# Kernel tuning notes

Measured on AMD Instinct MI355X. Metric: run time of the kernel, lower is better.

The kernel has to match this reference:

```python
import jax, jax.numpy as jnp
import numpy as np

OPTION_NUM = 5
HEADS = 4
NUM_LAYERS = 3
N_NODES = 20000
N_EDGES = 640000
NODES_PER_GRAPH = 800
N_GRAPHS = 25          # N_NODES // NODES_PER_GRAPH, multiple of OPTION_NUM
N_GROUPS = 5           # N_GRAPHS // OPTION_NUM; must equal OPTION_NUM for output_layer
T_TOK = 256
TOKEN_DIM = 1024
D = 256                # out_channels
VOCAB = 100000


def setup_inputs() -> dict:
    key = jax.random.key(0)
    ks = jax.random.split(key, 16)
    nrm = lambda k, s: jax.random.normal(k, s, dtype=jnp.float32) * 0.05
    L = NUM_LAYERS
    return {
        "concept_ids": jax.random.randint(ks[0], (N_NODES,), 0, VOCAB, dtype=jnp.int32),
        "edge_index": jax.random.randint(ks[1], (2, N_EDGES), 0, N_NODES, dtype=jnp.int32),
        "edge_type": jax.random.randint(ks[2], (N_EDGES,), 0, 38, dtype=jnp.int32),
        "sentence_embeddings": nrm(ks[3], (N_GROUPS, TOKEN_DIM)),
        "token_embedding": nrm(ks[4], (N_GROUPS, T_TOK, TOKEN_DIM)),
        "batch": (jnp.arange(N_NODES, dtype=jnp.int32) // NODES_PER_GRAPH),
        "entity_embeddings": nrm(ks[5], (VOCAB, D)),
        "Wq": nrm(ks[6], (L, D, D)), "bq": jnp.zeros((L, D), jnp.float32),
        "Wk": nrm(ks[7], (L, D, D)), "bk": jnp.zeros((L, D), jnp.float32),
        "Wv": nrm(ks[8], (L, D, D)), "bv": jnp.zeros((L, D), jnp.float32),
        "Ws": nrm(ks[9], (L, TOKEN_DIM, D)), "bs": jnp.zeros((L, D), jnp.float32),
        "Wo": nrm(ks[10], (L, D, D)), "bo": jnp.zeros((L, D), jnp.float32),
        "W1": nrm(ks[11], (D, D)), "b1": jnp.zeros((D,), jnp.float32),
        "W2": nrm(ks[12], (TOKEN_DIM, D)), "b2": jnp.zeros((D,), jnp.float32),
        "W3": nrm(ks[13], (D, TOKEN_DIM)), "b3": jnp.zeros((TOKEN_DIM,), jnp.float32),
        "Wout": nrm(ks[14], (OPTION_NUM * D, D)), "bout": jnp.zeros((D,), jnp.float32),
    }


def reference(concept_ids, edge_index, edge_type, sentence_embeddings, token_embedding,
              batch, entity_embeddings, Wq, bq, Wk, bk, Wv, bv, Ws, bs, Wo, bo,
              W1, b1, W2, b2, W3, b3, Wout, bout):
    H = HEADS
    C = D // H
    sqdk = jnp.sqrt(jnp.float32(C))
    group = batch // OPTION_NUM                      # [N] in [0, N_GROUPS)
    row, col = edge_index[0], edge_index[1]

    x = entity_embeddings[concept_ids]               # [N, D]
    for l in range(NUM_LAYERS):
        Q = (x @ Wq[l] + bq[l]).reshape(-1, H, C)
        K = (x @ Wk[l] + bk[l]).reshape(-1, H, C)
        V = (x @ Wv[l] + bv[l]).reshape(-1, H, C)
        QS = (sentence_embeddings[group] @ Ws[l] + bs[l]).reshape(-1, H, C)
        Qi, Kj = Q[row], K[col]                      # [E, H, C]
        alpha = ((Qi * Kj).sum(-1) + (QS[row] * Kj).sum(-1) + (Qi * QS[col]).sum(-1)) / (3.0 * sqdk)
        alpha = jax.nn.leaky_relu(alpha, 0.2)
        alpha = jax.nn.softmax(alpha, axis=0)        # global softmax over edges (as in source)
        agg = jnp.zeros_like(V).at[row].add(V[col] * alpha[:, :, None])
        x = agg.reshape(-1, H * C) @ Wo[l] + bo[l] + x

    x = x @ W1 + b1                                  # [N, D]
    tok = token_embedding @ W2 + b2                  # [G, T, D]

    # attention_multihead (faithful double gather by group indices)
    scale = jnp.sqrt(jnp.float32(D))
    scores = jnp.einsum('nd,btd->bnt', x, tok) / scale   # [G, N, T]
    sel = scores[:, group, :]                            # gather dim 1
    w = jax.nn.softmax(sel, axis=-1)
    ao = jnp.einsum('bnt,btd->bnd', w, tok)              # [G, N, D]
    sel2 = ao[:, group, :]                               # second gather
    concat = jnp.transpose(sel2, (1, 0, 2)).reshape(x.shape[0], -1)  # [N, G*D]
    x = concat @ Wout + bout                             # [N, D]

    pooled = jax.ops.segment_max(x, batch, num_segments=N_GRAPHS)    # global_max_pool
    soft = pooled @ W3 + b3                              # [N_GRAPHS, token_dim]
    return soft.reshape(N_GRAPHS // OPTION_NUM, OPTION_NUM, -1)
```

## Files before the change

kernel.cpp:

```cpp
#include <hip/hip_runtime.h>
#include <hip/hip_bf16.h>

#define NNODES 20000
#define NEDGES 640000
#define DM 256
#define PAD 128

typedef short s16x8 __attribute__((ext_vector_type(8)));
typedef float f32x4 __attribute__((ext_vector_type(4)));
typedef float f32x2 __attribute__((ext_vector_type(2)));

__device__ inline float b2f(unsigned short u) {
  union { unsigned int i; float f; } z;
  z.i = (unsigned int)u << 16;
  return z.f;
}
__device__ inline unsigned short f2b(float f) {
  union { unsigned int i; float f; } z;
  z.f = f;
  unsigned int i = z.i;
  return (unsigned short)((i + 0x7FFFu + ((i >> 16) & 1u)) >> 16);
}

__device__ inline unsigned char f2fp8(float v) {
#if __has_builtin(__builtin_amdgcn_cvt_pk_fp8_f32)
  int t = __builtin_amdgcn_cvt_pk_fp8_f32(v, v, 0, false);
  return (unsigned char)(t & 0xFF);
#else
  union { float f; unsigned int u; } z;
  z.f = v;
  unsigned int s = (z.u >> 31) << 7;
  float av = fabsf(v);
  if (av >= 448.f) return (unsigned char)(s | 0x7E);
  if (av < 0.015625f) {
    int q = (int)rintf(av * 512.f);
    return (unsigned char)(s | (unsigned)q);
  }
  int e32 = (int)((z.u >> 23) & 255) - 127;
  unsigned mant = z.u & 0x7FFFFF;
  unsigned t = mant + 0x7FFFF + ((mant >> 20) & 1);
  if (t >= 0x800000u) { t = 0; e32++; }
  int e4 = e32 + 7;
  unsigned m3 = (t >> 20) & 7;
  if (e4 > 15 || (e4 == 15 && m3 == 7)) return (unsigned char)(s | 0x7E);
  return (unsigned char)(s | (unsigned)((e4 << 3) | m3));
#endif
}

__device__ inline float4 fp8x4_dec(unsigned int u) {
#if __has_builtin(__builtin_amdgcn_cvt_pk_f32_fp8)
  f32x2 lo = __builtin_amdgcn_cvt_pk_f32_fp8((int)u, false);
  f32x2 hi = __builtin_amdgcn_cvt_pk_f32_fp8((int)u, true);
  float4 r;
  r.x = lo[0]; r.y = lo[1]; r.z = hi[0]; r.w = hi[1];
  return r;
#else
  float4 r;
  float* p = &r.x;
#pragma unroll
  for (int j = 0; j < 4; j++) {
    unsigned b = (u >> (8 * j)) & 0xFF;
    unsigned s = b >> 7, e = (b >> 3) & 15, m = b & 7;
    float mag;
    if (e == 0) mag = (float)m * 0.001953125f;
    else {
      union { unsigned int i; float f; } z;
      z.i = ((e + 120u) << 23) | (m << 20);
      mag = z.f;
    }
    p[j] = s ? -mag : mag;
  }
  return r;
#endif
}

__global__ __launch_bounds__(256) void init_kernel(
    const int* __restrict__ cid, const float* __restrict__ ent,
    float* __restrict__ x, unsigned short* __restrict__ xb,
    const float* __restrict__ Wq, const float* __restrict__ Wk,
    const float* __restrict__ Wv, const float* __restrict__ Wo,
    unsigned short* __restrict__ WT, const float* __restrict__ W2,
    unsigned short* __restrict__ W2T, const float* __restrict__ te,
    unsigned short* __restrict__ tb, const float* __restrict__ sent,
    const float* __restrict__ Ws, const float* __restrict__ bs,
    float* __restrict__ QS5all, const int* __restrict__ ei,
    const int* __restrict__ batch, int* __restrict__ deg,
    int* __restrict__ colPad) {
  int blk = blockIdx.x;
  int j = threadIdx.x;
  if (blk < 60) {
    int chunk = blk & 3;
    int lg = blk >> 2;
    int l = lg / 5, g = lg % 5;
    __shared__ float sh[256];
    sh[j] = sent[g * 1024 + chunk * 256 + j];
    __syncthreads();
    const float* W = Ws + (size_t)l * 1024 * 256 + (size_t)chunk * 256 * 256;
    float acc = (chunk == 0) ? bs[l * 256 + j] : 0.f;
#pragma unroll 8
    for (int k = 0; k < 256; k++) acc += sh[k] * W[k * 256 + j];
    atomicAdd(&QS5all[(size_t)lg * 256 + j], acc);
  } else if (blk < 2560) {
    int e = (blk - 60) * 256 + j;
    if (e >= NEDGES) return;
    int r = ei[e];
    int c = ei[NEDGES + e];
    int slot = atomicAdd(&deg[r], 1);
    if (slot < PAD)
      colPad[(size_t)r * PAD + slot] = c | ((batch[c] / 5) << 24);
  } else if (blk < 7560) {
    int idx = (blk - 2560) * 256 + j;
    if (idx >= NNODES * 64) return;
    int node = idx >> 6, d4 = idx & 63;
    float4 v =
        reinterpret_cast<const float4*>(ent)[(size_t)cid[node] * 64 + d4];
    reinterpret_cast<float4*>(x)[(size_t)node * 64 + d4] = v;
    ushort4 b;
    b.x = f2b(v.x); b.y = f2b(v.y); b.z = f2b(v.z); b.w = f2b(v.w);
    reinterpret_cast<ushort4*>(xb)[(size_t)node * 64 + d4] = b;
  } else if (blk < 10632) {
    int pblk = blk - 7560;
    int slot = pblk >> 8;
    int l = slot >> 2, t = slot & 3;
    int n = pblk & 255;
    const float* src = (t == 0) ? Wq : (t == 1) ? Wk : (t == 2) ? Wv : Wo;
    WT[(size_t)slot * 65536 + n * 256 + j] =
        f2b(src[(size_t)l * 65536 + j * 256 + n]);
  } else if (blk < 11656) {
    int i = (blk - 10632) * 256 + j;
    int n = i >> 10, k = i & 1023;
    W2T[n * 1024 + k] = f2b(W2[k * 256 + n]);
  } else {
    int i = (blk - 11656) * 256 + j;
    float4 v = reinterpret_cast<const float4*>(te)[i];
    ushort4 b;
    b.x = f2b(v.x); b.y = f2b(v.y); b.z = f2b(v.z); b.w = f2b(v.w);
    reinterpret_cast<ushort4*>(tb)[i] = b;
  }
}

template <int WITH_TOK>
__global__ __launch_bounds__(256) void qkv_gemm_kernel(
    const unsigned short* __restrict__ A, const unsigned short* __restrict__ Bt,
    const float* __restrict__ bq, const float* __restrict__ bk,
    const float* __restrict__ bv, unsigned short* __restrict__ Qb,
    unsigned char* __restrict__ KV8, int M,
    const unsigned short* __restrict__ tokA,
    const unsigned short* __restrict__ W2T, const float* __restrict__ b2,
    float* __restrict__ tokOut) {
  int wid = threadIdx.x >> 6;
  int lane = threadIdx.x & 63;
  int wr = wid >> 1, wc = wid & 1;
  int r16 = lane & 15, kg = lane >> 4;
  if (WITH_TOK && blockIdx.x >= 6) {
    if (blockIdx.y >= 20) return;
    int rowBase = blockIdx.y * 64 + wr * 32;
    int colBase = (blockIdx.x - 6) * 128 + wc * 64;
    f32x4 acc[2][4] = {};
    for (int k0 = 0; k0 < 1024; k0 += 32) {
      s16x8 a[2], b[4];
#pragma unroll
      for (int mi = 0; mi < 2; mi++) {
        int r = rowBase + mi * 16 + r16;
        a[mi] = *reinterpret_cast<const s16x8*>(
            &tokA[(size_t)r * 1024 + k0 + kg * 8]);
      }
#pragma unroll
      for (int ni = 0; ni < 4; ni++) {
        int c = colBase + ni * 16 + r16;
        b[ni] = *reinterpret_cast<const s16x8*>(
            &W2T[(size_t)c * 1024 + k0 + kg * 8]);
      }
#pragma unroll
      for (int mi = 0; mi < 2; mi++)
#pragma unroll
        for (int ni = 0; ni < 4; ni++)
          acc[mi][ni] = __builtin_amdgcn_mfma_f32_16x16x32_bf16(
              a[mi], b[ni], acc[mi][ni], 0, 0, 0);
    }
#pragma unroll
    for (int mi = 0; mi < 2; mi++)
#pragma unroll
      for (int ni = 0; ni < 4; ni++) {
        int c = colBase + ni * 16 + (lane & 15);
        float bia = b2[c];
#pragma unroll
        for (int reg = 0; reg < 4; reg++) {
          int r = rowBase + mi * 16 + (lane >> 4) * 4 + reg;
          tokOut[(size_t)r * 256 + c] = acc[mi][ni][reg] + bia;
        }
      }
    return;
  }
  int rowBase = blockIdx.y * 64 + wr * 32;
  int colBase = blockIdx.x * 128 + wc * 64;
  f32x4 acc[2][4] = {};
  for (int k0 = 0; k0 < 256; k0 += 32) {
    s16x8 a[2], b[4];
#pragma unroll
    for (int mi = 0; mi < 2; mi++) {
      int r = rowBase + mi * 16 + r16;
      s16x8 z = {};
      a[mi] = (r < M) ? *reinterpret_cast<const s16x8*>(
                            &A[(size_t)r * 256 + k0 + kg * 8])
                      : z;
    }
#pragma unroll
    for (int ni = 0; ni < 4; ni++) {
      int c = colBase + ni * 16 + r16;
      b[ni] = *reinterpret_cast<const s16x8*>(&Bt[(size_t)c * 256 + k0 + kg * 8]);
    }
#pragma unroll
    for (int mi = 0; mi < 2; mi++)
#pragma unroll
      for (int ni = 0; ni < 4; ni++)
        acc[mi][ni] = __builtin_amdgcn_mfma_f32_16x16x32_bf16(
            a[mi], b[ni], acc[mi][ni], 0, 0, 0);
  }
  int region = (blockIdx.x * 128) >> 8;
  const float* bias = (region == 0) ? bq : (region == 1) ? bk : bv;
  unsigned char* dstBase = KV8 + ((region == 1) ? 0 : 256);
#pragma unroll
  for (int mi = 0; mi < 2; mi++)
#pragma unroll
    for (int ni = 0; ni < 4; ni++) {
      int cg = colBase + ni * 16 + (lane & 15);
      int cr = cg & 255;
      float bia = bias[cr];
#pragma unroll
      for (int reg = 0; reg < 4; reg++) {
        int r = rowBase + mi * 16 + (lane >> 4) * 4 + reg;
        if (r >= M) continue;
        float v = acc[mi][ni][reg] + bia;
        if (region == 0)
          Qb[(size_t)r * 256 + cr] = f2b(v);
        else
          dstBase[(size_t)r * 512 + cr] = f2fp8(v);
      }
    }
}

__global__ __launch_bounds__(256) void gemm_bf16_kernel(
    const unsigned short* __restrict__ A, const unsigned short* __restrict__ Bt,
    const float* __restrict__ bias, const float* __restrict__ resid,
    float* __restrict__ Cf, unsigned short* __restrict__ Cb, int M, int K) {
  int wid = threadIdx.x >> 6;
  int lane = threadIdx.x & 63;
  int wr = wid >> 1, wc = wid & 1;
  int rowBase = blockIdx.y * 64 + wr * 32;
  int colBase = blockIdx.x * 128 + wc * 64;
  int r16 = lane & 15, kg = lane >> 4;
  f32x4 acc[2][4] = {};
  for (int k0 = 0; k0 < K; k0 += 32) {
    s16x8 a[2], b[4];
#pragma unroll
    for (int mi = 0; mi < 2; mi++) {
      int r = rowBase + mi * 16 + r16;
      s16x8 z = {};
      a[mi] = (r < M) ? *reinterpret_cast<const s16x8*>(
                            &A[(size_t)r * K + k0 + kg * 8])
                      : z;
    }
#pragma unroll
    for (int ni = 0; ni < 4; ni++) {
      int c = colBase + ni * 16 + r16;
      b[ni] = *reinterpret_cast<const s16x8*>(&Bt[(size_t)c * K + k0 + kg * 8]);
    }
#pragma unroll
    for (int mi = 0; mi < 2; mi++)
#pragma unroll
      for (int ni = 0; ni < 4; ni++)
        acc[mi][ni] = __builtin_amdgcn_mfma_f32_16x16x32_bf16(
            a[mi], b[ni], acc[mi][ni], 0, 0, 0);
  }
#pragma unroll
  for (int mi = 0; mi < 2; mi++)
#pragma unroll
    for (int ni = 0; ni < 4; ni++) {
      int c = colBase + ni * 16 + (lane & 15);
      float bia = bias[c];
#pragma unroll
      for (int reg = 0; reg < 4; reg++) {
        int r = rowBase + mi * 16 + (lane >> 4) * 4 + reg;
        if (r >= M) continue;
        float v = acc[mi][ni][reg] + bia;
        if (resid) v += resid[(size_t)r * 256 + c];
        if (Cf) Cf[(size_t)r * 256 + c] = v;
        if (Cb) Cb[(size_t)r * 256 + c] = f2b(v);
      }
    }
}

__global__ __launch_bounds__(256) void rescale_wo_kernel(
    unsigned short* __restrict__ WoT, const float* __restrict__ sums) {
  int i = blockIdx.x * 256 + threadIdx.x;
  int head = (i & 255) >> 6;
  WoT[i] = f2b(b2f(WoT[i]) / sums[head]);
}

template <int DO_AGG>
__global__ __launch_bounds__(256) void fused_edge_kernel(
    const int* __restrict__ deg, const int* __restrict__ colPad,
    const int* __restrict__ batch, const unsigned short* __restrict__ Qb,
    const unsigned int* __restrict__ KV, const float* __restrict__ QS5,
    float* __restrict__ sums, unsigned short* __restrict__ aggb, int n) {
  int wv = __builtin_amdgcn_readfirstlane(threadIdx.x >> 6);
  int node = blockIdx.x * 4 + wv;
  int lane = threadIdx.x & 63;
  int head = lane >> 4;
  float sum0 = 0.f, sum1 = 0.f, sum2 = 0.f, sum3 = 0.f;
  float4 a0 = {0.f, 0.f, 0.f, 0.f}, a1 = a0, a2 = a0, a3 = a0;
  float4 qe = a0;
  float dq0 = 0.f, dq1 = 0.f, dq2 = 0.f, dq3 = 0.f, dq4 = 0.f;
  int dcount = 0;
  if (node < n) {
    ushort4 qu =
        reinterpret_cast<const ushort4*>(Qb)[(size_t)node * 64 + lane];
    float4 q = {b2f(qu.x), b2f(qu.y), b2f(qu.z), b2f(qu.w)};
    int gr = batch[node] / 5;
    float4 qs = reinterpret_cast<const float4*>(QS5)[gr * 64 + lane];
    qe.x = q.x + qs.x; qe.y = q.y + qs.y; qe.z = q.z + qs.z; qe.w = q.w + qs.w;
#pragma unroll
    for (int g = 0; g < 5; g++) {
      float4 w = reinterpret_cast<const float4*>(QS5)[g * 64 + lane];
      float d = q.x * w.x + q.y * w.y + q.z * w.z + q.w * w.w;
      d += __shfl_xor(d, 1);
      d += __shfl_xor(d, 2);
      d += __shfl_xor(d, 4);
      d += __shfl_xor(d, 8);
      if (g == 0) dq0 = d;
      else if (g == 1) dq1 = d;
      else if (g == 2) dq2 = d;
      else if (g == 3) dq3 = d;
      else dq4 = d;
    }
    dcount = deg[node];
    if (dcount > PAD) dcount = PAD;
  }
  const int* myCol = colPad + (size_t)node * PAD;
  bool lead = (lane & 15) == 0;
  int m = 0;
  for (; m + 4 <= dcount; m += 4) {
    int cc0 = myCol[m + 0], cc1 = myCol[m + 1];
    int cc2 = myCol[m + 2], cc3 = myCol[m + 3];
    int c0 = cc0 & 0xFFFFFF, c1 = cc1 & 0xFFFFFF;
    int c2 = cc2 & 0xFFFFFF, c3 = cc3 & 0xFFFFFF;
    unsigned int kr0 = KV[(size_t)c0 * 128 + lane];
    unsigned int kr1 = KV[(size_t)c1 * 128 + lane];
    unsigned int kr2 = KV[(size_t)c2 * 128 + lane];
    unsigned int kr3 = KV[(size_t)c3 * 128 + lane];
    unsigned int vr0 = 0, vr1 = 0, vr2 = 0, vr3 = 0;
    if (DO_AGG) {
      vr0 = KV[(size_t)c0 * 128 + 64 + lane];
      vr1 = KV[(size_t)c1 * 128 + 64 + lane];
      vr2 = KV[(size_t)c2 * 128 + 64 + lane];
      vr3 = KV[(size_t)c3 * 128 + 64 + lane];
    }
    float4 kd0 = fp8x4_dec(kr0), kd1 = fp8x4_dec(kr1);
    float4 kd2 = fp8x4_dec(kr2), kd3 = fp8x4_dec(kr3);
    float p0 = qe.x * kd0.x + qe.y * kd0.y + qe.z * kd0.z + qe.w * kd0.w;
    float p1 = qe.x * kd1.x + qe.y * kd1.y + qe.z * kd1.z + qe.w * kd1.w;
    float p2 = qe.x * kd2.x + qe.y * kd2.y + qe.z * kd2.z + qe.w * kd2.w;
    float p3 = qe.x * kd3.x + qe.y * kd3.y + qe.z * kd3.z + qe.w * kd3.w;
    p0 += __shfl_xor(p0, 1); p1 += __shfl_xor(p1, 1);
    p2 += __shfl_xor(p2, 1); p3 += __shfl_xor(p3, 1);
    p0 += __shfl_xor(p0, 2); p1 += __shfl_xor(p1, 2);
    p2 += __shfl_xor(p2, 2); p3 += __shfl_xor(p3, 2);
    p0 += __shfl_xor(p0, 4); p1 += __shfl_xor(p1, 4);
    p2 += __shfl_xor(p2, 4); p3 += __shfl_xor(p3, 4);
    p0 += __shfl_xor(p0, 8); p1 += __shfl_xor(p1, 8);
    p2 += __shfl_xor(p2, 8); p3 += __shfl_xor(p3, 8);
    int gc0 = cc0 >> 24, gc1 = cc1 >> 24, gc2 = cc2 >> 24, gc3 = cc3 >> 24;
    float dv0 = (gc0 == 0) ? dq0 : (gc0 == 1) ? dq1 : (gc0 == 2) ? dq2 : (gc0 == 3) ? dq3 : dq4;
    float dv1 = (gc1 == 0) ? dq0 : (gc1 == 1) ? dq1 : (gc1 == 2) ? dq2 : (gc1 == 3) ? dq3 : dq4;
    float dv2 = (gc2 == 0) ? dq0 : (gc2 == 1) ? dq1 : (gc2 == 2) ? dq2 : (gc2 == 3) ? dq3 : dq4;
    float dv3 = (gc3 == 0) ? dq0 : (gc3 == 1) ? dq1 : (gc3 == 2) ? dq2 : (gc3 == 3) ? dq3 : dq4;
    float v0 = (p0 + dv0) * (1.f / 24.f); v0 = fmaxf(v0, 0.2f * v0);
    float v1 = (p1 + dv1) * (1.f / 24.f); v1 = fmaxf(v1, 0.2f * v1);
    float v2 = (p2 + dv2) * (1.f / 24.f); v2 = fmaxf(v2, 0.2f * v2);
    float v3 = (p3 + dv3) * (1.f / 24.f); v3 = fmaxf(v3, 0.2f * v3);
    float e0 = __expf(v0), e1 = __expf(v1), e2 = __expf(v2), e3 = __expf(v3);
    if (lead) { sum0 += e0; sum1 += e1; sum2 += e2; sum3 += e3; }
    if (DO_AGG) {
      float4 vd0 = fp8x4_dec(vr0), vd1 = fp8x4_dec(vr1);
      float4 vd2 = fp8x4_dec(vr2), vd3 = fp8x4_dec(vr3);
      a0.x += e0 * vd0.x; a0.y += e0 * vd0.y; a0.z += e0 * vd0.z; a0.w += e0 * vd0.w;
      a1.x += e1 * vd1.x; a1.y += e1 * vd1.y; a1.z += e1 * vd1.z; a1.w += e1 * vd1.w;
      a2.x += e2 * vd2.x; a2.y += e2 * vd2.y; a2.z += e2 * vd2.z; a2.w += e2 * vd2.w;
      a3.x += e3 * vd3.x; a3.y += e3 * vd3.y; a3.z += e3 * vd3.z; a3.w += e3 * vd3.w;
    }
  }
  for (; m < dcount; m++) {
    int cc = myCol[m];
    int c = cc & 0xFFFFFF, gc = cc >> 24;
    float4 kd = fp8x4_dec(KV[(size_t)c * 128 + lane]);
    float p = qe.x * kd.x + qe.y * kd.y + qe.z * kd.z + qe.w * kd.w;
    p += __shfl_xor(p, 1);
    p += __shfl_xor(p, 2);
    p += __shfl_xor(p, 4);
    p += __shfl_xor(p, 8);
    float dqv = (gc == 0) ? dq0 : (gc == 1) ? dq1 : (gc == 2) ? dq2
                : (gc == 3) ? dq3 : dq4;
    float v = (p + dqv) * (1.f / 24.f);
    v = fmaxf(v, 0.2f * v);
    float ev = __expf(v);
    if (lead) sum0 += ev;
    if (DO_AGG) {
      float4 vd = fp8x4_dec(KV[(size_t)c * 128 + 64 + lane]);
      a0.x += ev * vd.x; a0.y += ev * vd.y; a0.z += ev * vd.z; a0.w += ev * vd.w;
    }
  }
  float sumExp = (sum0 + sum1) + (sum2 + sum3);
  if (DO_AGG && node < n) {
    float4 acc;
    acc.x = (a0.x + a1.x) + (a2.x + a3.x);
    acc.y = (a0.y + a1.y) + (a2.y + a3.y);
    acc.z = (a0.z + a1.z) + (a2.z + a3.z);
    acc.w = (a0.w + a1.w) + (a2.w + a3.w);
    ushort4 b;
    b.x = f2b(acc.x); b.y = f2b(acc.y); b.z = f2b(acc.z); b.w = f2b(acc.w);
    reinterpret_cast<ushort4*>(aggb)[(size_t)node * 64 + lane] = b;
  }
  __shared__ float red[4][4];
  int w = threadIdx.x >> 6;
  if (lead) red[w][head] = sumExp;
  __syncthreads();
  if (threadIdx.x < 4) {
    float t = red[0][threadIdx.x] + red[1][threadIdx.x] + red[2][threadIdx.x] +
              red[3][threadIdx.x];
    atomicAdd(&sums[threadIdx.x], t);
  }
}

__global__ __launch_bounds__(1024) void tail_head_kernel(
    const int* __restrict__ deg, const int* __restrict__ colPad,
    const int* __restrict__ batch, const unsigned short* __restrict__ Qb,
    const unsigned int* __restrict__ KV, const unsigned short* __restrict__ xb,
    const float* __restrict__ QS5, const float* __restrict__ sums,
    const float* __restrict__ Wv2, const float* __restrict__ bv2,
    const float* __restrict__ Wo2, const float* __restrict__ bo2,
    const float* __restrict__ x, const float* __restrict__ W1,
    const float* __restrict__ b1, float* __restrict__ x1) {
  __shared__ float xh[4][256];
  __shared__ float sE4[4];
  __shared__ float a0s[256];
  __shared__ float t1[256];
  __shared__ float part[4][256];
  int tid = threadIdx.x;
  if (tid < 64) {
    int lane = tid;
    int head = lane >> 4;
    ushort4 qu = reinterpret_cast<const ushort4*>(Qb)[lane];
    float4 q = {b2f(qu.x), b2f(qu.y), b2f(qu.z), b2f(qu.w)};
    int gr = batch[0] / 5;
    float4 qs = reinterpret_cast<const float4*>(QS5)[gr * 64 + lane];
    float4 qe = {q.x + qs.x, q.y + qs.y, q.z + qs.z, q.w + qs.w};
    float dq0 = 0.f, dq1 = 0.f, dq2 = 0.f, dq3 = 0.f, dq4 = 0.f;
#pragma unroll
    for (int g = 0; g < 5; g++) {
      float4 w = reinterpret_cast<const float4*>(QS5)[g * 64 + lane];
      float d = q.x * w.x + q.y * w.y + q.z * w.z + q.w * w.w;
      d += __shfl_xor(d, 1);
      d += __shfl_xor(d, 2);
      d += __shfl_xor(d, 4);
      d += __shfl_xor(d, 8);
      if (g == 0) dq0 = d;
      else if (g == 1) dq1 = d;
      else if (g == 2) dq2 = d;
      else if (g == 3) dq3 = d;
      else dq4 = d;
    }
    float4 xaccA = {0, 0, 0, 0}, xaccB = xaccA, xaccC = xaccA, xaccD = xaccA;
    float sE = 0.f;
    int dcount = deg[0];
    if (dcount > PAD) dcount = PAD;
    for (int m = 0; m < dcount; m++) {
      int cc = colPad[m];
      int c = cc & 0xFFFFFF, gc = cc >> 24;
      float4 kd = fp8x4_dec(KV[(size_t)c * 128 + lane]);
      float p = qe.x * kd.x + qe.y * kd.y + qe.z * kd.z + qe.w * kd.w;
      p += __shfl_xor(p, 1);
      p += __shfl_xor(p, 2);
      p += __shfl_xor(p, 4);
      p += __shfl_xor(p, 8);
      float dqv = (gc == 0) ? dq0 : (gc == 1) ? dq1 : (gc == 2) ? dq2
                  : (gc == 3) ? dq3 : dq4;
      float v = (p + dqv) * (1.f / 24.f);
      v = fmaxf(v, 0.2f * v);
      float ev = __expf(v);
      sE += ev;
      float e0 = __shfl(ev, 0);
      float e1 = __shfl(ev, 16);
      float e2 = __shfl(ev, 32);
      float e3 = __shfl(ev, 48);
      ushort4 xu = reinterpret_cast<const ushort4*>(xb)[(size_t)c * 64 + lane];
      float4 xv = {b2f(xu.x), b2f(xu.y), b2f(xu.z), b2f(xu.w)};
      xaccA.x += e0 * xv.x; xaccA.y += e0 * xv.y; xaccA.z += e0 * xv.z; xaccA.w += e0 * xv.w;
      xaccB.x += e1 * xv.x; xaccB.y += e1 * xv.y; xaccB.z += e1 * xv.z; xaccB.w += e1 * xv.w;
      xaccC.x += e2 * xv.x; xaccC.y += e2 * xv.y; xaccC.z += e2 * xv.z; xaccC.w += e2 * xv.w;
      xaccD.x += e3 * xv.x; xaccD.y += e3 * xv.y; xaccD.z += e3 * xv.z; xaccD.w += e3 * xv.w;
    }
    xh[0][lane * 4 + 0] = xaccA.x; xh[0][lane * 4 + 1] = xaccA.y;
    xh[0][lane * 4 + 2] = xaccA.z; xh[0][lane * 4 + 3] = xaccA.w;
    xh[1][lane * 4 + 0] = xaccB.x; xh[1][lane * 4 + 1] = xaccB.y;
    xh[1][lane * 4 + 2] = xaccB.z; xh[1][lane * 4 + 3] = xaccB.w;
    xh[2][lane * 4 + 0] = xaccC.x; xh[2][lane * 4 + 1] = xaccC.y;
    xh[2][lane * 4 + 2] = xaccC.z; xh[2][lane * 4 + 3] = xaccC.w;
    xh[3][lane * 4 + 0] = xaccD.x; xh[3][lane * 4 + 1] = xaccD.y;
    xh[3][lane * 4 + 2] = xaccD.z; xh[3][lane * 4 + 3] = xaccD.w;
    if ((lane & 15) == 0) sE4[head] = sE;
  }
  __syncthreads();
  int j = tid & 255, s = tid >> 8;
  int hj = j >> 6;
  float accv = 0.f;
#pragma unroll 8
  for (int k = s * 64; k < s * 64 + 64; k++) accv += xh[hj][k] * Wv2[k * 256 + j];
  part[s][j] = accv;
  __syncthreads();
  if (tid < 256) {
    float tot = part[0][tid] + part[1][tid] + part[2][tid] + part[3][tid] +
                sE4[hj] * bv2[tid];
    a0s[tid] = tot / sums[hj];
  }
  __syncthreads();
  float acc = 0.f;
#pragma unroll 8
  for (int k = s * 64; k < s * 64 + 64; k++) acc += a0s[k] * Wo2[k * 256 + j];
  part[s][j] = acc;
  __syncthreads();
  if (tid < 256)
    t1[tid] = part[0][tid] + part[1][tid] + part[2][tid] + part[3][tid] +
              bo2[tid] + x[tid];
  __syncthreads();
  float acc2 = 0.f;
#pragma unroll 8
  for (int k = s * 64; k < s * 64 + 64; k++) acc2 += t1[k] * W1[k * 256 + j];
  part[s][j] = acc2;
  __syncthreads();
  if (tid < 256)
    x1[tid] = part[0][tid] + part[1][tid] + part[2][tid] + part[3][tid] +
              b1[tid];
}

__global__ __launch_bounds__(256) void attn_out_kernel(
    const float* __restrict__ x1g, const float* __restrict__ tok,
    float* __restrict__ AO) {
  int b = blockIdx.x;
  int tid = threadIdx.x;
  int wave = tid >> 6, lane = tid & 63;
  int sub = lane >> 4, l16 = lane & 15;
  __shared__ float x1s[256];
  __shared__ float scs[256];
  __shared__ float red[256];
  __shared__ float wgt[256];
  x1s[tid] = x1g[tid];
  __syncthreads();
  const float4* xv4 = reinterpret_cast<const float4*>(x1s);
  for (int it = 0; it < 16; it++) {
    int row = wave * 64 + it * 4 + sub;
    const float4* tr =
        reinterpret_cast<const float4*>(tok + (size_t)(b * 256 + row) * 256);
    float sc = 0.f;
#pragma unroll
    for (int q = 0; q < 4; q++) {
      float4 v = tr[l16 + q * 16];
      float4 xv = xv4[l16 + q * 16];
      sc += v.x * xv.x + v.y * xv.y + v.z * xv.z + v.w * xv.w;
    }
    sc += __shfl_xor(sc, 1);
    sc += __shfl_xor(sc, 2);
    sc += __shfl_xor(sc, 4);
    sc += __shfl_xor(sc, 8);
    if (l16 == 0) scs[row] = sc * (1.f / 16.f);
  }
  __syncthreads();
  float sc = scs[tid];
  red[tid] = sc;
  __syncthreads();
  for (int off = 128; off; off >>= 1) {
    if (tid < off) red[tid] = fmaxf(red[tid], red[tid + off]);
    __syncthreads();
  }
  float mx = red[0];
  __syncthreads();
  float ex = expf(sc - mx);
  red[tid] = ex;
  __syncthreads();
  for (int off = 128; off; off >>= 1) {
    if (tid < off) red[tid] += red[tid + off];
    __syncthreads();
  }
  wgt[tid] = ex / red[0];
  __syncthreads();
  float acc = 0.f;
#pragma unroll 4
  for (int k = 0; k < 256; k++)
    acc += wgt[k] * tok[(size_t)(b * 256 + k) * 256 + tid];
  AO[b * 256 + tid] = acc;
}

__global__ __launch_bounds__(256) void final_y_kernel(
    const float* __restrict__ AO, const float* __restrict__ Wout,
    float* __restrict__ partial) {
  int s = blockIdx.x;
  int j = threadIdx.x;
  __shared__ float a[80];
  if (threadIdx.x < 80) a[threadIdx.x] = AO[s * 80 + threadIdx.x];
  __syncthreads();
  const float* W = Wout + (size_t)s * 80 * 256;
  float acc = 0.f;
#pragma unroll 8
  for (int k = 0; k < 80; k++) acc += a[k] * W[k * 256 + j];
  partial[s * 256 + j] = acc;
}

__global__ __launch_bounds__(256) void final_out2_kernel(
    const float* __restrict__ partial, const float* __restrict__ bout,
    const float* __restrict__ W3, const float* __restrict__ b3,
    float* __restrict__ out) {
  __shared__ float y[256];
  int j = threadIdx.x;
  float acc = bout[j];
#pragma unroll
  for (int s = 0; s < 16; s++) acc += partial[s * 256 + j];
  y[j] = acc;
  __syncthreads();
  int t = blockIdx.x * 256 + j;
  float o = b3[t];
#pragma unroll 8
  for (int k = 0; k < 256; k++) o += y[k] * W3[k * 1024 + t];
  for (int g = 0; g < 25; g++) out[(size_t)g * 1024 + t] = o;
}

extern "C" void kernel_launch(void* const* d_in, const int* in_sizes, int n_in,
                              void* d_out, int out_size, void* d_ws,
                              size_t ws_size, hipStream_t stream) {
  const int* concept_ids = (const int*)d_in[0];
  const int* edge_index = (const int*)d_in[1];
  const float* sent = (const float*)d_in[3];
  const float* tokemb = (const float*)d_in[4];
  const int* batch = (const int*)d_in[5];
  const float* ent = (const float*)d_in[6];
  const float* Wq = (const float*)d_in[7];
  const float* bq = (const float*)d_in[8];
  const float* Wk = (const float*)d_in[9];
  const float* bk = (const float*)d_in[10];
  const float* Wv = (const float*)d_in[11];
  const float* bv = (const float*)d_in[12];
  const float* Ws = (const float*)d_in[13];
  const float* bs = (const float*)d_in[14];
  const float* Wo = (const float*)d_in[15];
  const float* bo = (const float*)d_in[16];
  const float* W1 = (const float*)d_in[17];
  const float* b1 = (const float*)d_in[18];
  const float* W2 = (const float*)d_in[19];
  const float* b2 = (const float*)d_in[20];
  const float* W3 = (const float*)d_in[21];
  const float* b3 = (const float*)d_in[22];
  const float* Wout = (const float*)d_in[23];
  const float* bout = (const float*)d_in[24];
  float* out = (float*)d_out;

  float* ws = (float*)d_ws;
  size_t off_ = 0;
  auto alloc = [&](size_t n) {
    float* p = ws + off_;
    off_ += n;
    return p;
  };
  float* x = alloc((size_t)NNODES * DM);
  float* x2 = alloc((size_t)NNODES * DM);
  unsigned short* Qb = (unsigned short*)alloc((size_t)NNODES * DM / 2);
  unsigned short* xb = (unsigned short*)alloc((size_t)NNODES * DM / 2);
  unsigned short* aggb = (unsigned short*)alloc((size_t)NNODES * DM / 2);
  unsigned char* KV8 = (unsigned char*)alloc((size_t)NNODES * DM / 2);
  unsigned short* WT = (unsigned short*)alloc(12 * 65536 / 2);
  unsigned short* W2T = (unsigned short*)alloc(262144 / 2);
  unsigned short* tokb = (unsigned short*)alloc(1280 * 1024 / 2);
  float* tok = alloc(1280 * 256);
  float* QS5all = alloc(3 * 5 * 256);
  float* sums = alloc(16);
  float* x1 = alloc(256);
  float* AO = alloc(1280);
  float* partial = alloc(16 * 256);
  int* deg = (int*)alloc(NNODES);
  int* colPad = (int*)alloc((size_t)NNODES * PAD);

  hipMemsetAsync(deg, 0, NNODES * sizeof(int), stream);
  hipMemsetAsync(sums, 0, 12 * sizeof(float), stream);
  hipMemsetAsync(QS5all, 0, 3 * 5 * 256 * sizeof(float), stream);
  init_kernel<<<12936, 256, 0, stream>>>(
      concept_ids, ent, x, xb, Wq, Wk, Wv, Wo, WT, W2, W2T, tokemb, tokb, sent,
      Ws, bs, QS5all, edge_index, batch, deg, colPad);

  float* xin = x;
  float* xout = x2;
  for (int l = 0; l < 3; l++) {
    unsigned short* WoT = WT + (size_t)(l * 4 + 3) * 65536;
    if (l == 0) {
      dim3 g(8, (NNODES + 63) / 64);
      qkv_gemm_kernel<1><<<g, 256, 0, stream>>>(
          xb, WT + (size_t)(l * 4) * 65536, bq + l * DM, bk + l * DM,
          bv + l * DM, Qb, KV8, NNODES, tokb, W2T, b2, tok);
    } else {
      dim3 g((l < 2) ? 6 : 4, (NNODES + 63) / 64);
      qkv_gemm_kernel<0><<<g, 256, 0, stream>>>(
          xb, WT + (size_t)(l * 4) * 65536, bq + l * DM, bk + l * DM,
          bv + l * DM, Qb, KV8, NNODES, nullptr, nullptr, nullptr, nullptr);
    }
    if (l < 2) {
      fused_edge_kernel<1><<<5000, 256, 0, stream>>>(
          deg, colPad, batch, Qb, (const unsigned int*)KV8, QS5all + l * 1280,
          sums + l * 4, aggb, NNODES);
      rescale_wo_kernel<<<256, 256, 0, stream>>>(WoT, sums + l * 4);
      dim3 g(2, (NNODES + 63) / 64);
      gemm_bf16_kernel<<<g, 256, 0, stream>>>(aggb, WoT, bo + l * DM, xin,
                                              xout, xb, NNODES, 256);
      float* tmp = xin;
      xin = xout;
      xout = tmp;
    } else {
      fused_edge_kernel<0><<<5000, 256, 0, stream>>>(
          deg, colPad, batch, Qb, (const unsigned int*)KV8, QS5all + l * 1280,
          sums + l * 4, nullptr, NNODES);
      tail_head_kernel<<<1, 1024, 0, stream>>>(
          deg, colPad, batch, Qb, (const unsigned int*)KV8, xb,
          QS5all + l * 1280, sums + l * 4, Wv + (size_t)2 * 65536,
          bv + 2 * DM, Wo + (size_t)2 * 65536, bo + 2 * DM, xin, W1, b1, x1);
    }
  }

  attn_out_kernel<<<5, 256, 0, stream>>>(x1, tok, AO);
  final_y_kernel<<<16, 256, 0, stream>>>(AO, Wout, partial);
  final_out2_kernel<<<4, 256, 0, stream>>>(partial, bout, W3, b3, out);
}
```

Measured before the change: 593.3 us.

## Bucket CSR adjacency by source-node chunk to localize KV gathers

Edge binning now splits each row's adjacency into four buckets by column-node range (5000 nodes each, up to 32 slots per bucket), with per-row per-bucket degree counters. The edge kernel walks the buckets in order, so successive gathers of K/V rows touch a narrower address range, aiming at better cache locality. Remainder edges now go through a masked 4-wide step instead of a scalar tail loop. This adds loop overhead and raises the overflow risk, since a bucket holding more than 32 edges drops edges where the old single 128-slot row would have kept them.

```diff
diff --git a/kernel.cpp b/kernel.cpp
--- a/kernel.cpp
+++ b/kernel.cpp
@@ -4,7 +4,8 @@
 #define NNODES 20000
 #define NEDGES 640000
 #define DM 256
-#define PAD 128
+#define CHW 5000
+#define CSL 32
 
 typedef short s16x8 __attribute__((ext_vector_type(8)));
 typedef float f32x4 __attribute__((ext_vector_type(4)));
@@ -84,7 +85,7 @@
     unsigned short* __restrict__ tb, const float* __restrict__ sent,
     const float* __restrict__ Ws, const float* __restrict__ bs,
     float* __restrict__ QS5all, const int* __restrict__ ei,
-    const int* __restrict__ batch, int* __restrict__ deg,
+    const int* __restrict__ batch, int* __restrict__ deg4,
     int* __restrict__ colPad) {
   int blk = blockIdx.x;
   int j = threadIdx.x;
@@ -105,9 +106,10 @@
     if (e >= NEDGES) return;
     int r = ei[e];
     int c = ei[NEDGES + e];
-    int slot = atomicAdd(&deg[r], 1);
-    if (slot < PAD)
-      colPad[(size_t)r * PAD + slot] = c | ((batch[c] / 5) << 24);
+    int ch = c / CHW;
+    int slot = atomicAdd(&deg4[r * 4 + ch], 1);
+    if (slot < CSL)
+      colPad[(size_t)r * 128 + ch * CSL + slot] = c | ((batch[c] / 5) << 24);
   } else if (blk < 7560) {
     int idx = (blk - 2560) * 256 + j;
     if (idx >= NNODES * 64) return;
@@ -300,7 +302,7 @@
 
 template <int DO_AGG>
 __global__ __launch_bounds__(256) void fused_edge_kernel(
-    const int* __restrict__ deg, const int* __restrict__ colPad,
+    const int* __restrict__ deg4, const int* __restrict__ colPad,
     const int* __restrict__ batch, const unsigned short* __restrict__ Qb,
     const unsigned int* __restrict__ KV, const float* __restrict__ QS5,
     float* __restrict__ sums, unsigned short* __restrict__ aggb, int n) {
@@ -312,7 +314,7 @@
   float4 a0 = {0.f, 0.f, 0.f, 0.f}, a1 = a0, a2 = a0, a3 = a0;
   float4 qe = a0;
   float dq0 = 0.f, dq1 = 0.f, dq2 = 0.f, dq3 = 0.f, dq4 = 0.f;
-  int dcount = 0;
+  int4 dd = {0, 0, 0, 0};
   if (node < n) {
     ushort4 qu =
         reinterpret_cast<const ushort4*>(Qb)[(size_t)node * 64 + lane];
@@ -334,82 +336,97 @@
       else if (g == 3) dq3 = d;
       else dq4 = d;
     }
-    dcount = deg[node];
-    if (dcount > PAD) dcount = PAD;
-  }
-  const int* myCol = colPad + (size_t)node * PAD;
+    dd = *reinterpret_cast<const int4*>(&deg4[node * 4]);
+  }
   bool lead = (lane & 15) == 0;
-  int m = 0;
-  for (; m + 4 <= dcount; m += 4) {
-    int cc0 = myCol[m + 0], cc1 = myCol[m + 1];
-    int cc2 = myCol[m + 2], cc3 = myCol[m + 3];
-    int c0 = cc0 & 0xFFFFFF, c1 = cc1 & 0xFFFFFF;
-    int c2 = cc2 & 0xFFFFFF, c3 = cc3 & 0xFFFFFF;
-    unsigned int kr0 = KV[(size_t)c0 * 128 + lane];
-    unsigned int kr1 = KV[(size_t)c1 * 128 + lane];
-    unsigned int kr2 = KV[(size_t)c2 * 128 + lane];
-    unsigned int kr3 = KV[(size_t)c3 * 128 + lane];
-    unsigned int vr0 = 0, vr1 = 0, vr2 = 0, vr3 = 0;
-    if (DO_AGG) {
-      vr0 = KV[(size_t)c0 * 128 + 64 + lane];
-      vr1 = KV[(size_t)c1 * 128 + 64 + lane];
-      vr2 = KV[(size_t)c2 * 128 + 64 + lane];
-      vr3 = KV[(size_t)c3 * 128 + 64 + lane];
-    }
-    float4 kd0 = fp8x4_dec(kr0), kd1 = fp8x4_dec(kr1);
-    float4 kd2 = fp8x4_dec(kr2), kd3 = fp8x4_dec(kr3);
-    float p0 = qe.x * kd0.x + qe.y * kd0.y + qe.z * kd0.z + qe.w * kd0.w;
-    float p1 = qe.x * kd1.x + qe.y * kd1.y + qe.z * kd1.z + qe.w * kd1.w;
-    float p2 = qe.x * kd2.x + qe.y * kd2.y + qe.z * kd2.z + qe.w * kd2.w;
-    float p3 = qe.x * kd3.x + qe.y * kd3.y + qe.z * kd3.z + qe.w * kd3.w;
-    p0 += __shfl_xor(p0, 1); p1 += __shfl_xor(p1, 1);
-    p2 += __shfl_xor(p2, 1); p3 += __shfl_xor(p3, 1);
-    p0 += __shfl_xor(p0, 2); p1 += __shfl_xor(p1, 2);
-    p2 += __shfl_xor(p2, 2); p3 += __shfl_xor(p3, 2);
-    p0 += __shfl_xor(p0, 4); p1 += __shfl_xor(p1, 4);
-    p2 += __shfl_xor(p2, 4); p3 += __shfl_xor(p3, 4);
-    p0 += __shfl_xor(p0, 8); p1 += __shfl_xor(p1, 8);
-    p2 += __shfl_xor(p2, 8); p3 += __shfl_xor(p3, 8);
-    int gc0 = cc0 >> 24, gc1 = cc1 >> 24, gc2 = cc2 >> 24, gc3 = cc3 >> 24;
-    float dv0 = (gc0 == 0) ? dq0 : (gc0 == 1) ? dq1 : (gc0 == 2) ? dq2 : (gc0 == 3) ? dq3 : dq4;
-    float dv1 = (gc1 == 0) ? dq0 : (gc1 == 1) ? dq1 : (gc1 == 2) ? dq2 : (gc1 == 3) ? dq3 : dq4;
-    float dv2 = (gc2 == 0) ? dq0 : (gc2 == 1) ? dq1 : (gc2 == 2) ? dq2 : (gc2 == 3) ? dq3 : dq4;
-    float dv3 = (gc3 == 0) ? dq0 : (gc3 == 1) ? dq1 : (gc3 == 2) ? dq2 : (gc3 == 3) ? dq3 : dq4;
-    float v0 = (p0 + dv0) * (1.f / 24.f); v0 = fmaxf(v0, 0.2f * v0);
-    float v1 = (p1 + dv1) * (1.f / 24.f); v1 = fmaxf(v1, 0.2f * v1);
-    float v2 = (p2 + dv2) * (1.f / 24.f); v2 = fmaxf(v2, 0.2f * v2);
-    float v3 = (p3 + dv3) * (1.f / 24.f); v3 = fmaxf(v3, 0.2f * v3);
-    float e0 = __expf(v0), e1 = __expf(v1), e2 = __expf(v2), e3 = __expf(v3);
-    if (lead) { sum0 += e0; sum1 += e1; sum2 += e2; sum3 += e3; }
-    if (DO_AGG) {
-      float4 vd0 = fp8x4_dec(vr0), vd1 = fp8x4_dec(vr1);
-      float4 vd2 = fp8x4_dec(vr2), vd3 = fp8x4_dec(vr3);
-      a0.x += e0 * vd0.x; a0.y += e0 * vd0.y; a0.z += e0 * vd0.z; a0.w += e0 * vd0.w;
-      a1.x += e1 * vd1.x; a1.y += e1 * vd1.y; a1.z += e1 * vd1.z; a1.w += e1 * vd1.w;
-      a2.x += e2 * vd2.x; a2.y += e2 * vd2.y; a2.z += e2 * vd2.z; a2.w += e2 * vd2.w;
-      a3.x += e3 * vd3.x; a3.y += e3 * vd3.y; a3.z += e3 * vd3.z; a3.w += e3 * vd3.w;
-    }
-  }
-  for (; m < dcount; m++) {
-    int cc = myCol[m];
-    int c = cc & 0xFFFFFF, gc = cc >> 24;
-    float4 kd = fp8x4_dec(KV[(size_t)c * 128 + lane]);
-    float p = qe.x * kd.x + qe.y * kd.y + qe.z * kd.z + qe.w * kd.w;
-    p += __shfl_xor(p, 1);
-    p += __shfl_xor(p, 2);
-    p += __shfl_xor(p, 4);
-    p += __shfl_xor(p, 8);
-    float dqv = (gc == 0) ? dq0 : (gc == 1) ? dq1 : (gc == 2) ? dq2
-                : (gc == 3) ? dq3 : dq4;
-    float v = (p + dqv) * (1.f / 24.f);
-    v = fmaxf(v, 0.2f * v);
-    float ev = __expf(v);
-    if (lead) sum0 += ev;
-    if (DO_AGG) {
-      float4 vd = fp8x4_dec(KV[(size_t)c * 128 + 64 + lane]);
-      a0.x += ev * vd.x; a0.y += ev * vd.y; a0.z += ev * vd.z; a0.w += ev * vd.w;
-    }
-  }
+
+#define EDGE4(MBASE, MASKED)                                                   \
+  {                                                                            \
+    int i0 = (MBASE), i1 = (MBASE) + 1, i2 = (MBASE) + 2, i3 = (MBASE) + 3;    \
+    bool v0_ = MASKED ? (i0 < dcount) : true;                                  \
+    bool v1_ = MASKED ? (i1 < dcount) : true;                                  \
+    bool v2_ = MASKED ? (i2 < dcount) : true;                                  \
+    bool v3_ = MASKED ? (i3 < dcount) : true;                                  \
+    int cc0 = v0_ ? myCol[i0] : 0;                                             \
+    int cc1 = v1_ ? myCol[i1] : 0;                                             \
+    int cc2 = v2_ ? myCol[i2] : 0;                                             \
+    int cc3 = v3_ ? myCol[i3] : 0;                                             \
+    int c0 = cc0 & 0xFFFFFF, c1 = cc1 & 0xFFFFFF;                              \
+    int c2 = cc2 & 0xFFFFFF, c3 = cc3 & 0xFFFFFF;                              \
+    unsigned int kr0 = KV[(size_t)c0 * 128 + lane];                            \
+    unsigned int kr1 = KV[(size_t)c1 * 128 + lane];                            \
+    unsigned int kr2 = KV[(size_t)c2 * 128 + lane];                            \
+    unsigned int kr3 = KV[(size_t)c3 * 128 + lane];                            \
+    unsigned int vr0 = 0, vr1 = 0, vr2 = 0, vr3 = 0;                           \
+    if (DO_AGG) {                                                              \
+      vr0 = KV[(size_t)c0 * 128 + 64 + lane];                                  \
+      vr1 = KV[(size_t)c1 * 128 + 64 + lane];                                  \
+      vr2 = KV[(size_t)c2 * 128 + 64 + lane];                                  \
+      vr3 = KV[(size_t)c3 * 128 + 64 + lane];                                  \
+    }                                                                          \
+    float4 kd0 = fp8x4_dec(kr0), kd1 = fp8x4_dec(kr1);                         \
+    float4 kd2 = fp8x4_dec(kr2), kd3 = fp8x4_dec(kr3);                         \
+    float p0 = qe.x * kd0.x + qe.y * kd0.y + qe.z * kd0.z + qe.w * kd0.w;      \
+    float p1 = qe.x * kd1.x + qe.y * kd1.y + qe.z * kd1.z + qe.w * kd1.w;      \
+    float p2 = qe.x * kd2.x + qe.y * kd2.y + qe.z * kd2.z + qe.w * kd2.w;      \
+    float p3 = qe.x * kd3.x + qe.y * kd3.y + qe.z * kd3.z + qe.w * kd3.w;      \
+    p0 += __shfl_xor(p0, 1); p1 += __shfl_xor(p1, 1);                          \
+    p2 += __shfl_xor(p2, 1); p3 += __shfl_xor(p3, 1);                          \
+    p0 += __shfl_xor(p0, 2); p1 += __shfl_xor(p1, 2);                          \
+    p2 += __shfl_xor(p2, 2); p3 += __shfl_xor(p3, 2);                          \
+    p0 += __shfl_xor(p0, 4); p1 += __shfl_xor(p1, 4);                          \
+    p2 += __shfl_xor(p2, 4); p3 += __shfl_xor(p3, 4);                          \
+    p0 += __shfl_xor(p0, 8); p1 += __shfl_xor(p1, 8);                          \
+    p2 += __shfl_xor(p2, 8); p3 += __shfl_xor(p3, 8);                          \
+    int gc0 = cc0 >> 24, gc1 = cc1 >> 24, gc2 = cc2 >> 24, gc3 = cc3 >> 24;    \
+    float dv0 = (gc0 == 0) ? dq0 : (gc0 == 1) ? dq1 : (gc0 == 2) ? dq2         \
+                : (gc0 == 3) ? dq3 : dq4;                                      \
+    float dv1 = (gc1 == 0) ? dq0 : (gc1 == 1) ? dq1 : (gc1 == 2) ? dq2         \
+                : (gc1 == 3) ? dq3 : dq4;                                      \
+    float dv2 = (gc2 == 0) ? dq0 : (gc2 == 1) ? dq1 : (gc2 == 2) ? dq2         \
+                : (gc2 == 3) ? dq3 : dq4;                                      \
+    float dv3 = (gc3 == 0) ? dq0 : (gc3 == 1) ? dq1 : (gc3 == 2) ? dq2         \
+                : (gc3 == 3) ? dq3 : dq4;                                      \
+    float s0_ = (p0 + dv0) * (1.f / 24.f); s0_ = fmaxf(s0_, 0.2f * s0_);       \
+    float s1_ = (p1 + dv1) * (1.f / 24.f); s1_ = fmaxf(s1_, 0.2f * s1_);       \
+    float s2_ = (p2 + dv2) * (1.f / 24.f); s2_ = fmaxf(s2_, 0.2f * s2_);       \
+    float s3_ = (p3 + dv3) * (1.f / 24.f); s3_ = fmaxf(s3_, 0.2f * s3_);       \
+    float e0 = __expf(s0_), e1 = __expf(s1_), e2 = __expf(s2_), e3 = __expf(s3_); \
+    if (MASKED) {                                                              \
+      if (!v0_) e0 = 0.f;                                                      \
+      if (!v1_) e1 = 0.f;                                                      \
+      if (!v2_) e2 = 0.f;                                                      \
+      if (!v3_) e3 = 0.f;                                                      \
+    }                                                                          \
+    if (lead) { sum0 += e0; sum1 += e1; sum2 += e2; sum3 += e3; }              \
+    if (DO_AGG) {                                                              \
+      float4 vd0 = fp8x4_dec(vr0), vd1 = fp8x4_dec(vr1);                       \
+      float4 vd2 = fp8x4_dec(vr2), vd3 = fp8x4_dec(vr3);                       \
+      a0.x += e0 * vd0.x; a0.y += e0 * vd0.y; a0.z += e0 * vd0.z;              \
+      a0.w += e0 * vd0.w;                                                      \
+      a1.x += e1 * vd1.x; a1.y += e1 * vd1.y; a1.z += e1 * vd1.z;              \
+      a1.w += e1 * vd1.w;                                                      \
+      a2.x += e2 * vd2.x; a2.y += e2 * vd2.y; a2.z += e2 * vd2.z;              \
+      a2.w += e2 * vd2.w;                                                      \
+      a3.x += e3 * vd3.x; a3.y += e3 * vd3.y; a3.z += e3 * vd3.z;              \
+      a3.w += e3 * vd3.w;                                                      \
+    }                                                                          \
+  }
+
+  for (int ch = 0; ch < 4; ch++) {
+    int dcount = (ch == 0) ? dd.x : (ch == 1) ? dd.y : (ch == 2) ? dd.z : dd.w;
+    if (dcount > CSL) dcount = CSL;
+    const int* myCol = colPad + (size_t)node * 128 + ch * CSL;
+    int m = 0;
+    for (; m + 4 <= dcount; m += 4) {
+      EDGE4(m, false)
+    }
+    if (m < dcount) {
+      EDGE4(m, true)
+    }
+  }
+#undef EDGE4
+
   float sumExp = (sum0 + sum1) + (sum2 + sum3);
   if (DO_AGG && node < n) {
     float4 acc;
@@ -433,7 +450,7 @@
 }
 
 __global__ __launch_bounds__(1024) void tail_head_kernel(
-    const int* __restrict__ deg, const int* __restrict__ colPad,
+    const int* __restrict__ deg4, const int* __restrict__ colPad,
     const int* __restrict__ batch, const unsigned short* __restrict__ Qb,
     const unsigned int* __restrict__ KV, const unsigned short* __restrict__ xb,
     const float* __restrict__ QS5, const float* __restrict__ sums,
@@ -472,33 +489,37 @@
     }
     float4 xaccA = {0, 0, 0, 0}, xaccB = xaccA, xaccC = xaccA, xaccD = xaccA;
     float sE = 0.f;
-    int dcount = deg[0];
-    if (dcount > PAD) dcount = PAD;
-    for (int m = 0; m < dcount; m++) {
-      int cc = colPad[m];
-      int c = cc & 0xFFFFFF, gc = cc >> 24;
-      float4 kd = fp8x4_dec(KV[(size_t)c * 128 + lane]);
-      float p = qe.x * kd.x + qe.y * kd.y + qe.z * kd.z + qe.w * kd.w;
-      p += __shfl_xor(p, 1);
-      p += __shfl_xor(p, 2);
-      p += __shfl_xor(p, 4);
-      p += __shfl_xor(p, 8);
-      float dqv = (gc == 0) ? dq0 : (gc == 1) ? dq1 : (gc == 2) ? dq2
-                  : (gc == 3) ? dq3 : dq4;
-      float v = (p + dqv) * (1.f / 24.f);
-      v = fmaxf(v, 0.2f * v);
-      float ev = __expf(v);
-      sE += ev;
-      float e0 = __shfl(ev, 0);
-      float e1 = __shfl(ev, 16);
-      float e2 = __shfl(ev, 32);
-      float e3 = __shfl(ev, 48);
-      ushort4 xu = reinterpret_cast<const ushort4*>(xb)[(size_t)c * 64 + lane];
-      float4 xv = {b2f(xu.x), b2f(xu.y), b2f(xu.z), b2f(xu.w)};
-      xaccA.x += e0 * xv.x; xaccA.y += e0 * xv.y; xaccA.z += e0 * xv.z; xaccA.w += e0 * xv.w;
-      xaccB.x += e1 * xv.x; xaccB.y += e1 * xv.y; xaccB.z += e1 * xv.z; xaccB.w += e1 * xv.w;
-      xaccC.x += e2 * xv.x; xaccC.y += e2 * xv.y; xaccC.z += e2 * xv.z; xaccC.w += e2 * xv.w;
-      xaccD.x += e3 * xv.x; xaccD.y += e3 * xv.y; xaccD.z += e3 * xv.z; xaccD.w += e3 * xv.w;
+    for (int ch = 0; ch < 4; ch++) {
+      int dcount = deg4[ch];
+      if (dcount > CSL) dcount = CSL;
+      const int* myCol = colPad + ch * CSL;
+      for (int m = 0; m < dcount; m++) {
+        int cc = myCol[m];
+        int c = cc & 0xFFFFFF, gc = cc >> 24;
+        float4 kd = fp8x4_dec(KV[(size_t)c * 128 + lane]);
+        float p = qe.x * kd.x + qe.y * kd.y + qe.z * kd.z + qe.w * kd.w;
+        p += __shfl_xor(p, 1);
+        p += __shfl_xor(p, 2);
+        p += __shfl_xor(p, 4);
+        p += __shfl_xor(p, 8);
+        float dqv = (gc == 0) ? dq0 : (gc == 1) ? dq1 : (gc == 2) ? dq2
+                    : (gc == 3) ? dq3 : dq4;
+        float v = (p + dqv) * (1.f / 24.f);
+        v = fmaxf(v, 0.2f * v);
+        float ev = __expf(v);
+        sE += ev;
+        float e0 = __shfl(ev, 0);
+        float e1 = __shfl(ev, 16);
+        float e2 = __shfl(ev, 32);
+        float e3 = __shfl(ev, 48);
+        ushort4 xu =
+            reinterpret_cast<const ushort4*>(xb)[(size_t)c * 64 + lane];
+        float4 xv = {b2f(xu.x), b2f(xu.y), b2f(xu.z), b2f(xu.w)};
+        xaccA.x += e0 * xv.x; xaccA.y += e0 * xv.y; xaccA.z += e0 * xv.z; xaccA.w += e0 * xv.w;
+        xaccB.x += e1 * xv.x; xaccB.y += e1 * xv.y; xaccB.z += e1 * xv.z; xaccB.w += e1 * xv.w;
+        xaccC.x += e2 * xv.x; xaccC.y += e2 * xv.y; xaccC.z += e2 * xv.z; xaccC.w += e2 * xv.w;
+        xaccD.x += e3 * xv.x; xaccD.y += e3 * xv.y; xaccD.z += e3 * xv.z; xaccD.w += e3 * xv.w;
+      }
     }
     xh[0][lane * 4 + 0] = xaccA.x; xh[0][lane * 4 + 1] = xaccA.y;
     xh[0][lane * 4 + 2] = xaccA.z; xh[0][lane * 4 + 3] = xaccA.w;
@@ -684,15 +705,15 @@
   float* x1 = alloc(256);
   float* AO = alloc(1280);
   float* partial = alloc(16 * 256);
-  int* deg = (int*)alloc(NNODES);
-  int* colPad = (int*)alloc((size_t)NNODES * PAD);
-
-  hipMemsetAsync(deg, 0, NNODES * sizeof(int), stream);
+  int* deg4 = (int*)alloc((size_t)NNODES * 4);
+  int* colPad = (int*)alloc((size_t)NNODES * 128);
+
+  hipMemsetAsync(deg4, 0, (size_t)NNODES * 4 * sizeof(int), stream);
   hipMemsetAsync(sums, 0, 12 * sizeof(float), stream);
   hipMemsetAsync(QS5all, 0, 3 * 5 * 256 * sizeof(float), stream);
   init_kernel<<<12936, 256, 0, stream>>>(
       concept_ids, ent, x, xb, Wq, Wk, Wv, Wo, WT, W2, W2T, tokemb, tokb, sent,
-      Ws, bs, QS5all, edge_index, batch, deg, colPad);
+      Ws, bs, QS5all, edge_index, batch, deg4, colPad);
 
   float* xin = x;
   float* xout = x2;
@@ -711,7 +732,7 @@
     }
     if (l < 2) {
       fused_edge_kernel<1><<<5000, 256, 0, stream>>>(
-          deg, colPad, batch, Qb, (const unsigned int*)KV8, QS5all + l * 1280,
+          deg4, colPad, batch, Qb, (const unsigned int*)KV8, QS5all + l * 1280,
           sums + l * 4, aggb, NNODES);
       rescale_wo_kernel<<<256, 256, 0, stream>>>(WoT, sums + l * 4);
       dim3 g(2, (NNODES + 63) / 64);
@@ -722,10 +743,10 @@
       xout = tmp;
     } else {
       fused_edge_kernel<0><<<5000, 256, 0, stream>>>(
-          deg, colPad, batch, Qb, (const unsigned int*)KV8, QS5all + l * 1280,
+          deg4, colPad, batch, Qb, (const unsigned int*)KV8, QS5all + l * 1280,
           sums + l * 4, nullptr, NNODES);
       tail_head_kernel<<<1, 1024, 0, stream>>>(
-          deg, colPad, batch, Qb, (const unsigned int*)KV8, xb,
+          deg4, colPad, batch, Qb, (const unsigned int*)KV8, xb,
           QS5all + l * 1280, sums + l * 4, Wv + (size_t)2 * 65536,
           bv + 2 * DM, Wo + (size_t)2 * 65536, bo + 2 * DM, xin, W1, b1, x1);
     }
```

After: 597.6 us. No clear change (+0.7%).
